# Optimization experiments

Measured on AMD Instinct MI355X. Metric: run time of the kernel, lower is better.

## Reference

```python
import jax, jax.numpy as jnp
import numpy as np

NUM_HEADS = 16
TEMPERATURE = 1.0


def setup_inputs() -> dict:
    key = jax.random.key(0)
    ks = jax.random.split(key, 6)
    B, H = 2048, 2048
    return {
        "hidden_states": jax.random.normal(ks[0], (B, H), dtype=jnp.float32),
        "attention_mask": jnp.ones((B,), dtype=bool),
        "Wq": jax.random.normal(ks[1], (H, H), dtype=jnp.float32) * 0.02,
        "Wk": jax.random.normal(ks[2], (H, H), dtype=jnp.float32) * 0.02,
        "Wv": jax.random.normal(ks[3], (H, H), dtype=jnp.float32) * 0.02,
        "Wo": jax.random.normal(ks[4], (H, H), dtype=jnp.float32) * 0.02,
        "scale_param": jnp.full((1,), -3.0, dtype=jnp.float32),
    }


def reference(hidden_states, attention_mask, Wq, Wk, Wv, Wo, scale_param):
    B, H = hidden_states.shape
    nh = NUM_HEADS
    hd = H // nh
    # projections (torch Linear: x @ W.T), reshape to [heads, batch, head_dim]
    q = (hidden_states @ Wq.T).reshape(B, nh, hd).transpose(1, 0, 2)
    k = (hidden_states @ Wk.T).reshape(B, nh, hd).transpose(1, 0, 2)
    v = (hidden_states @ Wv.T).reshape(B, nh, hd).transpose(1, 0, 2)
    # cross-batch scores [heads, B, B]
    scores = jnp.einsum('hqd,hkd->hqk', q, k) / (hd ** 0.5 * TEMPERATURE)
    neg_inf = jnp.float32(-jnp.inf)
    eye = jnp.eye(B, dtype=bool)  # exclude self-attention (diagonal)
    scores = jnp.where(eye[None, :, :], neg_inf, scores)
    scores = jnp.where(attention_mask[None, None, :], scores, neg_inf)
    attn = jax.nn.softmax(scores, axis=-1)
    attn = jnp.nan_to_num(attn, nan=0.0)  # rows fully masked -> 0 (dropout=0 is identity)
    ctx = jnp.einsum('hqk,hkd->hqd', attn, v)  # [heads, B, head_dim]
    ctx = ctx.transpose(1, 0, 2).reshape(B, H)
    cross = ctx @ Wo.T
    scale = jax.nn.sigmoid(scale_param[0])
    return hidden_states + scale * cross
```

## Files before the change

kernel.cpp:

```cpp
#include <hip/hip_runtime.h>

typedef __bf16 bf16;
typedef __attribute__((ext_vector_type(8))) __bf16 bf16x8;
typedef __attribute__((ext_vector_type(4))) float f32x4;
typedef __attribute__((ext_vector_type(4))) short s16x4;

#define HDIM 2048

__device__ __forceinline__ void glds16(const void* g, void* l) {
  __builtin_amdgcn_global_load_lds((const __attribute__((address_space(1))) void*)g,
                                   (__attribute__((address_space(3))) void*)l,
                                   16, 0, 0);
}

#define MFMA16(a, b, c) __builtin_amdgcn_mfma_f32_16x16x32_bf16(a, b, c, 0, 0, 0)

__global__ __launch_bounds__(256) void cvt5(
    const float* __restrict__ s0, const float* __restrict__ s1,
    const float* __restrict__ s2, const float* __restrict__ s3,
    const float* __restrict__ s4,
    bf16* __restrict__ d0, bf16* __restrict__ d1, bf16* __restrict__ d2,
    bf16* __restrict__ d3, bf16* __restrict__ d4) {
  const float* s; bf16* d;
  switch (blockIdx.y) {
    case 0: s = s0; d = d0; break;
    case 1: s = s1; d = d1; break;
    case 2: s = s2; d = d2; break;
    case 3: s = s3; d = d3; break;
    default: s = s4; d = d4; break;
  }
  const size_t base = (size_t)blockIdx.x * 4096 + (threadIdx.x << 2);
  for (int i = 0; i < 4; i++) {
    const float4 v = *(const float4*)(s + base + i * 1024);
    union { bf16 h[4]; s16x4 s4v; } u;
    u.h[0] = (bf16)v.x; u.h[1] = (bf16)v.y; u.h[2] = (bf16)v.z; u.h[3] = (bf16)v.w;
    *(s16x4*)(d + base + i * 1024) = u.s4v;
  }
}

__device__ __forceinline__ void gemm128_core(const bf16* __restrict__ A,
                                             const bf16* __restrict__ B,
                                             int rowBase, int colBase,
                                             f32x4 acc[4][4],
                                             bf16* ldsA, bf16* ldsB) {
  const int t = threadIdx.x;
  const int w = t >> 6, l = t & 63;
  const int wr = (w >> 1) << 6, wc = (w & 1) << 6;
  const int lr = l & 15, lq = l >> 4;

  for (int mi = 0; mi < 4; mi++)
    for (int ni = 0; ni < 4; ni++)
      for (int r = 0; r < 4; r++) acc[mi][ni][r] = 0.f;

  const int sRow = (w << 4) + (l >> 2);
  const int sCol = (l & 3) << 3;
  const bf16* gA = A + (size_t)(rowBase + sRow) * HDIM + sCol;
  const bf16* gB = B + (size_t)(colBase + sRow) * HDIM + sCol;
  bf16* lA = ldsA + (w << 9);
  bf16* lB = ldsB + (w << 9);

  for (int k0 = 0; k0 < HDIM; k0 += 32) {
    glds16(gA, lA);
    glds16(gA + (size_t)64 * HDIM, lA + 2048);
    glds16(gB, lB);
    glds16(gB + (size_t)64 * HDIM, lB + 2048);
    gA += 32; gB += 32;
    __syncthreads();

    bf16x8 af[4], bfr[4];
    for (int mi = 0; mi < 4; mi++)
      af[mi] = *(const bf16x8*)&ldsA[(wr + mi * 16 + lr) * 32 + lq * 8];
    for (int ni = 0; ni < 4; ni++)
      bfr[ni] = *(const bf16x8*)&ldsB[(wc + ni * 16 + lr) * 32 + lq * 8];
    for (int mi = 0; mi < 4; mi++)
      for (int ni = 0; ni < 4; ni++)
        acc[mi][ni] = MFMA16(af[mi], bfr[ni], acc[mi][ni]);
    __syncthreads();
  }
}

__global__ __launch_bounds__(256) void qkv_gemm(
    const bf16* __restrict__ hs, const bf16* __restrict__ Wq,
    const bf16* __restrict__ Wk, const bf16* __restrict__ Wv,
    bf16* __restrict__ qb, bf16* __restrict__ Kf, bf16* __restrict__ Vf) {
  __shared__ bf16 ldsA[128 * 32];
  __shared__ bf16 ldsB[128 * 32];
  const int z = blockIdx.z;
  const bf16* W = (z == 0) ? Wq : (z == 1) ? Wk : Wv;
  const int rowBase = blockIdx.y << 7, colBase = blockIdx.x << 7;
  f32x4 acc[4][4];
  gemm128_core(hs, W, rowBase, colBase, acc, ldsA, ldsB);

  const int t = threadIdx.x;
  const int w = t >> 6, l = t & 63;
  const int wr = (w >> 1) << 6, wc = (w & 1) << 6;
  const int lr = l & 15, lq = l >> 4;

  if (z == 0) {
    for (int mi = 0; mi < 4; mi++)
      for (int ni = 0; ni < 4; ni++) {
        const int col = colBase + wc + ni * 16 + lr;
        const int row0 = rowBase + wr + mi * 16 + lq * 4;
        for (int r = 0; r < 4; r++)
          qb[(size_t)(row0 + r) * HDIM + col] = (bf16)acc[mi][ni][r];
      }
  } else if (z == 1) {
    for (int mi = 0; mi < 4; mi++)
      for (int ni = 0; ni < 4; ni++) {
        const int dim = colBase + wc + ni * 16 + lr;
        const int hh = dim >> 7, ks = (dim >> 5) & 3, kh = (dim >> 3) & 3, j = dim & 7;
        const int row0 = rowBase + wr + mi * 16 + lq * 4;
        for (int r = 0; r < 4; r++) {
          const int key = row0 + r;
          const int kbk = key >> 7, kni = (key >> 4) & 7, kl = key & 15;
          Kf[(((size_t)hh * 16 + kbk) * 32 + kni * 4 + ks) * 512 +
             (kh * 16 + kl) * 8 + j] = (bf16)acc[mi][ni][r];
        }
      }
  } else {
    for (int mi = 0; mi < 4; mi++)
      for (int ni = 0; ni < 4; ni++) {
        const int dim = colBase + wc + ni * 16 + lr;
        const int hh = dim >> 7, vni = (dim >> 4) & 7, ll = dim & 15;
        const int row0 = rowBase + wr + mi * 16 + lq * 4;
        const int kbk = row0 >> 7, ks = (row0 >> 5) & 3, lh = (row0 >> 3) & 3;
        const int j0 = row0 & 7;
        union { bf16 h4[4]; s16x4 v; } u;
        for (int r = 0; r < 4; r++) u.h4[r] = (bf16)acc[mi][ni][r];
        *(s16x4*)&Vf[(((size_t)hh * 16 + kbk) * 32 + vni * 4 + ks) * 512 +
                     (lh * 16 + ll) * 8 + j0] = u.v;
      }
  }
}

__global__ __launch_bounds__(256, 1) void attn_kernel(
    const bf16* __restrict__ qb, const bf16* __restrict__ Kf,
    const bf16* __restrict__ Vf, const unsigned char* __restrict__ amask,
    bf16* __restrict__ ctx) {
  __shared__ bf16 Kl[32 * 512];
  __shared__ bf16 Vl[32 * 512];
  __shared__ bf16 Pl[4 * 32 * 64];

  const int qt = blockIdx.x, h = blockIdx.y;
  const int t = threadIdx.x, w = t >> 6, l = t & 63;
  const int lr = l & 15, lq = l >> 4;
  bf16* Pw = Pl + (w << 11);

  bf16x8 aq[2][4];
  for (int mi = 0; mi < 2; mi++)
    for (int ks = 0; ks < 4; ks++)
      aq[mi][ks] = *(const bf16x8*)&qb[(size_t)(qt * 128 + w * 32 + mi * 16 + lr) * HDIM +
                                       h * 128 + ks * 32 + lq * 8];

  f32x4 o[2][8];
  for (int mi = 0; mi < 2; mi++)
    for (int ni = 0; ni < 8; ni++)
      for (int r = 0; r < 4; r++) o[mi][ni][r] = 0.f;
  float lsum[2][4];
  for (int mi = 0; mi < 2; mi++)
    for (int r = 0; r < 4; r++) lsum[mi][r] = 0.f;

  const float c = 0.08838834764831845f * 1.4426950408889634f;

  const size_t headOff = (size_t)h * 16 * 32 * 512;
  bf16x8 vtmp[8];
  for (int i = 0; i < 8; i++) {
    const int frag = i * 4 + w;
    glds16(Kf + headOff + frag * 512 + l * 8, Kl + frag * 512);
  }
  for (int i = 0; i < 8; i++) {
    const int frag = i * 4 + w;
    vtmp[i] = *(const bf16x8*)&Vf[headOff + frag * 512 + l * 8];
  }

  for (int kbk = 0; kbk < 16; kbk++) {
    __syncthreads();

    for (int i = 0; i < 8; i++) {
      const int frag = i * 4 + w;
      *(bf16x8*)&Vl[frag * 512 + l * 8] = vtmp[i];
    }

    f32x4 s[2][8];
    for (int mi = 0; mi < 2; mi++)
      for (int ni = 0; ni < 8; ni++)
        for (int r = 0; r < 4; r++) s[mi][ni][r] = 0.f;
    for (int ks = 0; ks < 4; ks++) {
      bf16x8 bk[8];
      for (int ni = 0; ni < 8; ni++)
        bk[ni] = *(const bf16x8*)&Kl[(ni * 4 + ks) * 512 + l * 8];
      for (int ni = 0; ni < 8; ni++) {
        s[0][ni] = MFMA16(aq[0][ks], bk[ni], s[0][ni]);
        s[1][ni] = MFMA16(aq[1][ks], bk[ni], s[1][ni]);
      }
    }

    __syncthreads();

    if (kbk < 15) {
      const size_t tileOffN = headOff + (size_t)(kbk + 1) * 32 * 512;
      for (int i = 0; i < 8; i++) {
        const int frag = i * 4 + w;
        glds16(Kf + tileOffN + frag * 512 + l * 8, Kl + frag * 512);
      }
      for (int i = 0; i < 8; i++) {
        const int frag = i * 4 + w;
        vtmp[i] = *(const bf16x8*)&Vf[tileOffN + frag * 512 + l * 8];
      }
    }

    float am[8];
    for (int ni = 0; ni < 8; ni++)
      am[ni] = amask[kbk * 128 + ni * 16 + lr] ? 0.f : -1e30f;
    if (kbk == qt) {
      for (int mi = 0; mi < 2; mi++)
        for (int ni = 0; ni < 8; ni++) {
          const int colL = ni * 16 + lr;
          for (int r = 0; r < 4; r++) {
            const int rowL = w * 32 + mi * 16 + lq * 4 + r;
            float p = __builtin_exp2f(s[mi][ni][r] * c + am[ni]);
            if (colL == rowL) p = 0.f;
            s[mi][ni][r] = p;
            lsum[mi][r] += p;
          }
        }
    } else {
      for (int mi = 0; mi < 2; mi++)
        for (int ni = 0; ni < 8; ni++)
          for (int r = 0; r < 4; r++) {
            const float p = __builtin_exp2f(s[mi][ni][r] * c + am[ni]);
            s[mi][ni][r] = p;
            lsum[mi][r] += p;
          }
    }

    for (int p = 0; p < 2; p++) {
      for (int mi = 0; mi < 2; mi++)
        for (int nip = 0; nip < 4; nip++) {
          const int ni = p * 4 + nip;
          for (int r = 0; r < 4; r++) {
            const int rl = lq * 4 + r;
            Pw[(mi * 16 + rl) * 64 + (((nip * 2 + (lr >> 3)) ^ (rl & 7)) << 3) +
               (lr & 7)] = (bf16)s[mi][ni][r];
          }
        }
      for (int ksp = 0; ksp < 2; ksp++) {
        const int ks = p * 2 + ksp;
        bf16x8 bv[8];
        for (int ni = 0; ni < 8; ni++)
          bv[ni] = *(const bf16x8*)&Vl[(ni * 4 + ks) * 512 + l * 8];
        const int rchunk = ((ksp * 4 + lq) ^ (lr & 7)) << 3;
        const bf16x8 ap0 = *(const bf16x8*)&Pw[lr * 64 + rchunk];
        const bf16x8 ap1 = *(const bf16x8*)&Pw[(16 + lr) * 64 + rchunk];
        for (int ni = 0; ni < 8; ni++) {
          o[0][ni] = MFMA16(ap0, bv[ni], o[0][ni]);
          o[1][ni] = MFMA16(ap1, bv[ni], o[1][ni]);
        }
      }
    }
  }

  for (int mi = 0; mi < 2; mi++)
    for (int r = 0; r < 4; r++)
      for (int off = 1; off < 16; off <<= 1)
        lsum[mi][r] += __shfl_xor(lsum[mi][r], off);

  for (int mi = 0; mi < 2; mi++)
    for (int ni = 0; ni < 8; ni++)
      for (int r = 0; r < 4; r++) {
        const int row = qt * 128 + w * 32 + mi * 16 + lq * 4 + r;
        const int col = h * 128 + ni * 16 + lr;
        const float li = lsum[mi][r];
        ctx[(size_t)row * HDIM + col] = (bf16)((li > 0.f) ? o[mi][ni][r] / li : 0.f);
      }
}

__global__ __launch_bounds__(256) void out_gemm(
    const bf16* __restrict__ ctx, const bf16* __restrict__ Wo,
    const float* __restrict__ hs, const float* __restrict__ scale_p,
    float* __restrict__ outp) {
  __shared__ bf16 ldsA[128 * 32];
  __shared__ bf16 ldsB[64 * 32];
  const int rowBase = blockIdx.y << 7, colBase = blockIdx.x << 6;
  const int t = threadIdx.x;
  const int w = t >> 6, l = t & 63;
  const int wr = (w >> 1) << 6, wc = (w & 1) << 5;
  const int lr = l & 15, lq = l >> 4;

  f32x4 acc[4][2];
  for (int mi = 0; mi < 4; mi++)
    for (int ni = 0; ni < 2; ni++)
      for (int r = 0; r < 4; r++) acc[mi][ni][r] = 0.f;

  const int sRow = (w << 4) + (l >> 2);
  const int sCol = (l & 3) << 3;
  const bf16* gA = ctx + (size_t)(rowBase + sRow) * HDIM + sCol;
  const bf16* gB = Wo + (size_t)(colBase + sRow) * HDIM + sCol;
  bf16* lA = ldsA + (w << 9);
  bf16* lB = ldsB + (w << 9);

  for (int k0 = 0; k0 < HDIM; k0 += 32) {
    glds16(gA, lA);
    glds16(gA + (size_t)64 * HDIM, lA + 2048);
    glds16(gB, lB);
    gA += 32; gB += 32;
    __syncthreads();

    bf16x8 af[4], bfr[2];
    for (int mi = 0; mi < 4; mi++)
      af[mi] = *(const bf16x8*)&ldsA[(wr + mi * 16 + lr) * 32 + lq * 8];
    for (int ni = 0; ni < 2; ni++)
      bfr[ni] = *(const bf16x8*)&ldsB[(wc + ni * 16 + lr) * 32 + lq * 8];
    for (int mi = 0; mi < 4; mi++)
      for (int ni = 0; ni < 2; ni++)
        acc[mi][ni] = MFMA16(af[mi], bfr[ni], acc[mi][ni]);
    __syncthreads();
  }

  const float sig = 1.0f / (1.0f + __expf(-scale_p[0]));
  for (int mi = 0; mi < 4; mi++)
    for (int ni = 0; ni < 2; ni++) {
      const int col = colBase + wc + ni * 16 + lr;
      const int row0 = rowBase + wr + mi * 16 + lq * 4;
      for (int r = 0; r < 4; r++) {
        const size_t idx = (size_t)(row0 + r) * HDIM + col;
        outp[idx] = hs[idx] + sig * acc[mi][ni][r];
      }
    }
}

extern "C" void kernel_launch(void* const* d_in, const int* in_sizes, int n_in,
                              void* d_out, int out_size, void* d_ws, size_t ws_size,
                              hipStream_t stream) {
  const float* hs = (const float*)d_in[0];
  const unsigned char* amask = (const unsigned char*)d_in[1];
  const float* Wq = (const float*)d_in[2];
  const float* Wk = (const float*)d_in[3];
  const float* Wv = (const float*)d_in[4];
  const float* Wo = (const float*)d_in[5];
  const float* scale_p = (const float*)d_in[6];
  float* outp = (float*)d_out;

  const size_t N = (size_t)HDIM * HDIM;
  bf16* qb   = (bf16*)d_ws;
  bf16* Kf   = qb + N;
  bf16* Vf   = Kf + N;
  bf16* ctx  = Vf + N;
  bf16* hs16 = ctx + N;
  bf16* Wq16 = hs16 + N;
  bf16* Wk16 = Wq16 + N;
  bf16* Wv16 = Wk16 + N;
  bf16* Wo16 = Wv16 + N;

  cvt5<<<dim3(1024, 5), 256, 0, stream>>>(hs, Wq, Wk, Wv, Wo,
                                          hs16, Wq16, Wk16, Wv16, Wo16);
  qkv_gemm<<<dim3(16, 16, 3), 256, 0, stream>>>(hs16, Wq16, Wk16, Wv16, qb, Kf, Vf);
  attn_kernel<<<dim3(16, 16), 256, 0, stream>>>(qb, Kf, Vf, amask, ctx);
  out_gemm<<<dim3(32, 16), 256, 0, stream>>>(ctx, Wo16, hs, scale_p, outp);
}
```

Measured before the change: 290.8 us.

## Split attention over key range and merge partial sums in combine kernel

```diff
diff --git a/kernel.cpp b/kernel.cpp
--- a/kernel.cpp
+++ b/kernel.cpp
@@ -136,12 +136,12 @@
 __global__ __launch_bounds__(256, 1) void attn_kernel(
     const bf16* __restrict__ qb, const bf16* __restrict__ Kf,
     const bf16* __restrict__ Vf, const unsigned char* __restrict__ amask,
-    bf16* __restrict__ ctx) {
+    float* __restrict__ Of, float* __restrict__ lsumBuf) {
   __shared__ bf16 Kl[32 * 512];
   __shared__ bf16 Vl[32 * 512];
   __shared__ bf16 Pl[4 * 32 * 64];
 
-  const int qt = blockIdx.x, h = blockIdx.y;
+  const int qt = blockIdx.x, h = blockIdx.y, kk = blockIdx.z;
   const int t = threadIdx.x, w = t >> 6, l = t & 63;
   const int lr = l & 15, lq = l >> 4;
   bf16* Pw = Pl + (w << 11);
@@ -163,17 +163,19 @@
   const float c = 0.08838834764831845f * 1.4426950408889634f;
 
   const size_t headOff = (size_t)h * 16 * 32 * 512;
+  const size_t t0Off = headOff + (size_t)(kk * 8) * 32 * 512;
   bf16x8 vtmp[8];
   for (int i = 0; i < 8; i++) {
     const int frag = i * 4 + w;
-    glds16(Kf + headOff + frag * 512 + l * 8, Kl + frag * 512);
+    glds16(Kf + t0Off + frag * 512 + l * 8, Kl + frag * 512);
   }
   for (int i = 0; i < 8; i++) {
     const int frag = i * 4 + w;
-    vtmp[i] = *(const bf16x8*)&Vf[headOff + frag * 512 + l * 8];
-  }
-
-  for (int kbk = 0; kbk < 16; kbk++) {
+    vtmp[i] = *(const bf16x8*)&Vf[t0Off + frag * 512 + l * 8];
+  }
+
+  for (int tt = 0; tt < 8; tt++) {
+    const int kbk = kk * 8 + tt;
     __syncthreads();
 
     for (int i = 0; i < 8; i++) {
@@ -197,7 +199,7 @@
 
     __syncthreads();
 
-    if (kbk < 15) {
+    if (tt < 7) {
       const size_t tileOffN = headOff + (size_t)(kbk + 1) * 32 * 512;
       for (int i = 0; i < 8; i++) {
         const int frag = i * 4 + w;
@@ -265,14 +267,47 @@
       for (int off = 1; off < 16; off <<= 1)
         lsum[mi][r] += __shfl_xor(lsum[mi][r], off);
 
+  const size_t obase = (size_t)kk * ((size_t)HDIM * HDIM);
   for (int mi = 0; mi < 2; mi++)
     for (int ni = 0; ni < 8; ni++)
       for (int r = 0; r < 4; r++) {
         const int row = qt * 128 + w * 32 + mi * 16 + lq * 4 + r;
         const int col = h * 128 + ni * 16 + lr;
-        const float li = lsum[mi][r];
-        ctx[(size_t)row * HDIM + col] = (bf16)((li > 0.f) ? o[mi][ni][r] / li : 0.f);
-      }
+        Of[obase + (size_t)row * HDIM + col] = o[mi][ni][r];
+      }
+  if (lr == 0)
+    for (int mi = 0; mi < 2; mi++)
+      for (int r = 0; r < 4; r++) {
+        const int row = qt * 128 + w * 32 + mi * 16 + lq * 4 + r;
+        lsumBuf[((size_t)kk * 16 + h) * 2048 + row] = lsum[mi][r];
+      }
+}
+
+__global__ __launch_bounds__(256) void combine_kernel(
+    const float* __restrict__ Of, const float* __restrict__ lsumBuf,
+    bf16* __restrict__ ctx) {
+  const size_t base = (size_t)blockIdx.x * 2048 + ((size_t)threadIdx.x << 3);
+  const int row = (int)(base >> 11);
+  const int h = ((int)base & 2047) >> 7;
+  const float lt = lsumBuf[h * 2048 + row] + lsumBuf[(16 + h) * 2048 + row];
+  const float linv = (lt > 0.f) ? 1.f / lt : 0.f;
+  const float* p0 = Of + base;
+  const float* p1 = Of + (size_t)4194304 + base;
+  const float4 a0 = *(const float4*)p0;
+  const float4 a1 = *(const float4*)(p0 + 4);
+  const float4 b0 = *(const float4*)p1;
+  const float4 b1 = *(const float4*)(p1 + 4);
+  union { bf16 hh[8]; s16x4 v[2]; } u;
+  u.hh[0] = (bf16)((a0.x + b0.x) * linv);
+  u.hh[1] = (bf16)((a0.y + b0.y) * linv);
+  u.hh[2] = (bf16)((a0.z + b0.z) * linv);
+  u.hh[3] = (bf16)((a0.w + b0.w) * linv);
+  u.hh[4] = (bf16)((a1.x + b1.x) * linv);
+  u.hh[5] = (bf16)((a1.y + b1.y) * linv);
+  u.hh[6] = (bf16)((a1.z + b1.z) * linv);
+  u.hh[7] = (bf16)((a1.w + b1.w) * linv);
+  *(s16x4*)(ctx + base) = u.v[0];
+  *(s16x4*)(ctx + base + 4) = u.v[1];
 }
 
 __global__ __launch_bounds__(256) void out_gemm(
@@ -351,10 +386,13 @@
   bf16* Wk16 = Wq16 + N;
   bf16* Wv16 = Wk16 + N;
   bf16* Wo16 = Wv16 + N;
+  float* Of = (float*)hs16;
+  float* lsumBuf = (float*)d_out;
 
   cvt5<<<dim3(1024, 5), 256, 0, stream>>>(hs, Wq, Wk, Wv, Wo,
                                           hs16, Wq16, Wk16, Wv16, Wo16);
   qkv_gemm<<<dim3(16, 16, 3), 256, 0, stream>>>(hs16, Wq16, Wk16, Wv16, qb, Kf, Vf);
-  attn_kernel<<<dim3(16, 16), 256, 0, stream>>>(qb, Kf, Vf, amask, ctx);
+  attn_kernel<<<dim3(16, 16, 2), 256, 0, stream>>>(qb, Kf, Vf, amask, Of, lsumBuf);
+  combine_kernel<<<dim3(2048), 256, 0, stream>>>(Of, lsumBuf, ctx);
   out_gemm<<<dim3(32, 16), 256, 0, stream>>>(ctx, Wo16, hs, scale_p, outp);
 }
```

After: 309.0 us. 6.3% more time.
